# Optimization experiments

Hardware: AMD Instinct MI355X
Metric: run time of the kernel (lower is better)

## Reference

```python
import jax, jax.numpy as jnp
import numpy as np

B, S, H, D = 32, 2048, 1024, 1024
NEG_BIG = -1e10  # matches torch's -10000000000.0 sentinel


def setup_inputs() -> dict:
    key = jax.random.key(0)
    k1, k2, k3, k4, k5 = jax.random.split(key, 5)
    hidden = jax.random.normal(k1, (B, H), dtype=jnp.float32)
    encoder_outs = jax.random.normal(k2, (B, S, D), dtype=jnp.float32)
    src_lens = jax.random.randint(k3, (B,), 1, S + 1, dtype=jnp.int64 if jax.config.jax_enable_x64 else jnp.int32)
    W1 = jax.random.normal(k4, (D, H), dtype=jnp.float32) * (1.0 / np.sqrt(H))
    W2 = jax.random.normal(k5, (D, H + D), dtype=jnp.float32) * (1.0 / np.sqrt(H + D))
    return {"hidden": hidden, "encoder_outs": encoder_outs, "src_lens": src_lens, "W1": W1, "W2": W2}


def reference(hidden, encoder_outs, src_lens, W1, W2):
    # x = l1(hidden): (B, D)
    x = hidden @ W1.T
    # att_score: (B, S) (torch computes (S, B); we keep batch-major and transpose attn at the end)
    scores = jnp.einsum('bsd,bd->bs', encoder_outs, x)
    seq_len = encoder_outs.shape[1]
    mask = (jnp.arange(seq_len)[None, :] < src_lens[:, None]).astype(scores.dtype)  # (B, S)
    masked = mask * scores
    # torch quirk: exact zeros (masked OR genuinely-zero scores) -> -1e10
    masked = jnp.where(masked == 0.0, jnp.asarray(NEG_BIG, masked.dtype), masked)
    attn = jax.nn.softmax(masked, axis=1)  # softmax over seq dim (torch dim=0 of (S,B))
    ctx = jnp.einsum('bs,bsd->bd', attn, encoder_outs)  # weighted sum: (B, D)
    out = jnp.tanh(jnp.concatenate([ctx, hidden], axis=1) @ W2.T)  # (B, D)
    return out, attn.T  # attn returned as (S, B) to match torch
```

## Files before the change

kernel.cpp:

```cpp
#include <hip/hip_runtime.h>
#include <hip/hip_bf16.h>
#include <math.h>

#define BB 32
#define SS 2048
#define HH 1024
#define DD 1024
#define HD 2048
#define NSPLIT 32
#define KSPLIT 8
#define NEG_BIG -1e10f

__device__ __forceinline__ float wave_reduce_sum(float v) {
#pragma unroll
    for (int off = 32; off > 0; off >>= 1) v += __shfl_xor(v, off, 64);
    return v;
}

__device__ __forceinline__ float dot4(float4 a, float4 b) {
    return a.x * b.x + a.y * b.y + a.z * b.z + a.w * b.w;
}

__global__ __launch_bounds__(256) void k1_gemv_x(const float* __restrict__ hidden,
                                                 const float* __restrict__ W1,
                                                 float* __restrict__ x) {
    __shared__ float4 hs[16 * 256];
    int tid = threadIdx.x;
    int w = tid >> 6, lane = tid & 63;
    int d = blockIdx.x * 4 + w;
    const float4* wp = (const float4*)(W1 + (size_t)d * HH);
    float4 w0 = wp[lane], w1 = wp[lane + 64], w2 = wp[lane + 128], w3 = wp[lane + 192];
    const float4* hp = (const float4*)hidden;

    for (int half = 0; half < 2; ++half) {
        __syncthreads();
#pragma unroll
        for (int i = 0; i < 16; ++i) hs[i * 256 + tid] = hp[half * 4096 + i * 256 + tid];
        __syncthreads();
#pragma unroll 4
        for (int bl = 0; bl < 16; ++bl) {
            const float4* hb = hs + bl * 256;
            float s = dot4(hb[lane], w0) + dot4(hb[lane + 64], w1) +
                      dot4(hb[lane + 128], w2) + dot4(hb[lane + 192], w3);
            s = wave_reduce_sum(s);
            if (lane == 0) x[(half * 16 + bl) * DD + d] = s;
        }
    }
}

__global__ __launch_bounds__(512) void k2_fused(const float* __restrict__ enc,
                                                const float* __restrict__ x,
                                                const int* __restrict__ src_lens,
                                                float* __restrict__ scores,
                                                float* __restrict__ ctxp,
                                                float* __restrict__ m_part,
                                                float* __restrict__ l_part) {
    int b = blockIdx.x >> 5;
    int sp = blockIdx.x & 31;
    int tid = threadIdx.x;
    int w = tid >> 6, lane = tid & 63;
    int len = src_lens[b];
    int srow = sp * 64 + w * 8;

    float m = NEG_BIG, l = 0.f;
    float4 a0 = {0, 0, 0, 0}, a1 = {0, 0, 0, 0}, a2 = {0, 0, 0, 0}, a3 = {0, 0, 0, 0};

    if (srow < len) {
        const float4* xp = (const float4*)(x + (size_t)b * DD);
        float4 x0 = xp[lane], x1 = xp[lane + 64], x2 = xp[lane + 128], x3 = xp[lane + 192];
        int rend = min(8, len - srow);
        for (int r = 0; r < rend; ++r) {
            int s = srow + r;
            const float4* ep = (const float4*)(enc + ((size_t)b * SS + s) * DD);
            float4 e0 = ep[lane], e1 = ep[lane + 64], e2 = ep[lane + 128], e3 = ep[lane + 192];
            float part = dot4(e0, x0) + dot4(e1, x1) + dot4(e2, x2) + dot4(e3, x3);
            part = wave_reduce_sum(part);
            float v = part;
            if (v == 0.0f) v = NEG_BIG;
            if (lane == 0) scores[b * SS + s] = v;
            if (v > m) {
                float sc = __expf(m - v);
                m = v;
                l *= sc;
                a0.x *= sc; a0.y *= sc; a0.z *= sc; a0.w *= sc;
                a1.x *= sc; a1.y *= sc; a1.z *= sc; a1.w *= sc;
                a2.x *= sc; a2.y *= sc; a2.z *= sc; a2.w *= sc;
                a3.x *= sc; a3.y *= sc; a3.z *= sc; a3.w *= sc;
            }
            float p = __expf(v - m);
            l += p;
            a0.x += p * e0.x; a0.y += p * e0.y; a0.z += p * e0.z; a0.w += p * e0.w;
            a1.x += p * e1.x; a1.y += p * e1.y; a1.z += p * e1.z; a1.w += p * e1.w;
            a2.x += p * e2.x; a2.y += p * e2.y; a2.z += p * e2.z; a2.w += p * e2.w;
            a3.x += p * e3.x; a3.y += p * e3.y; a3.z += p * e3.z; a3.w += p * e3.w;
        }
    }
    {
        int s0 = max(srow, len);
        for (int s = s0 + lane; s < srow + 8; s += 64) scores[b * SS + s] = NEG_BIG;
    }

    __shared__ float4 lctx[8][256];
    __shared__ float lm[8], ll[8];
    lctx[w][lane] = a0;
    lctx[w][lane + 64] = a1;
    lctx[w][lane + 128] = a2;
    lctx[w][lane + 192] = a3;
    if (lane == 0) { lm[w] = m; ll[w] = l; }
    __syncthreads();

    if (tid < 256) {
        float M = lm[0];
#pragma unroll
        for (int k = 1; k < 8; ++k) M = fmaxf(M, lm[k]);
        float L = 0.f;
        float4 sum = {0, 0, 0, 0};
#pragma unroll
        for (int k = 0; k < 8; ++k) {
            float sc = __expf(lm[k] - M);
            L += sc * ll[k];
            float4 c = lctx[k][tid];
            sum.x += sc * c.x; sum.y += sc * c.y; sum.z += sc * c.z; sum.w += sc * c.w;
        }
        int cc = ((tid >> 6) << 8) | ((tid & 63) << 2);
        *(float4*)(ctxp + ((size_t)(b * NSPLIT + sp)) * DD + cc) = sum;
        if (tid == 0) {
            m_part[b * NSPLIT + sp] = M;
            l_part[b * NSPLIT + sp] = L;
        }
    }
}

__global__ __launch_bounds__(256) void k3_combine(const float* __restrict__ ctxp,
                                                  const float* __restrict__ m_part,
                                                  const float* __restrict__ l_part,
                                                  float* __restrict__ ctx,
                                                  float* __restrict__ Mb,
                                                  float* __restrict__ Lb) {
    int b = blockIdx.x;
    int tid = threadIdx.x;
    float M = -INFINITY;
#pragma unroll
    for (int k = 0; k < NSPLIT; ++k) M = fmaxf(M, m_part[b * NSPLIT + k]);
    float L = 0.f;
    float4 sum = {0, 0, 0, 0};
#pragma unroll
    for (int k = 0; k < NSPLIT; ++k) {
        float sc = __expf(m_part[b * NSPLIT + k] - M);
        L += sc * l_part[b * NSPLIT + k];
        float4 c = *(const float4*)(ctxp + ((size_t)(b * NSPLIT + k)) * DD + tid * 4);
        sum.x += sc * c.x; sum.y += sc * c.y; sum.z += sc * c.z; sum.w += sc * c.w;
    }
    float rL = 1.0f / L;
    float4 o = {sum.x * rL, sum.y * rL, sum.z * rL, sum.w * rL};
    *(float4*)(ctx + (size_t)b * DD + tid * 4) = o;
    if (tid == 0) { Mb[b] = M; Lb[b] = L; }
}

__global__ __launch_bounds__(256) void k5_outgemm(const float* __restrict__ ctx,
                                                  const float* __restrict__ hidden,
                                                  const float* __restrict__ W2,
                                                  float* __restrict__ outp) {
    int dt = blockIdx.x & 31;
    int ks = blockIdx.x >> 5;
    int tid = threadIdx.x;
    __shared__ float cat_s[32 * 128];
    __shared__ float w2_s[32 * 128];
    int b0 = tid & 15, b1 = b0 + 16;
    int dl0 = (tid >> 4) * 2, dl1 = dl0 + 1;
    float acc00 = 0.f, acc01 = 0.f, acc10 = 0.f, acc11 = 0.f;

    for (int c = 0; c < 2; ++c) {
        int j0 = ks * 256 + c * 128;
        __syncthreads();
#pragma unroll
        for (int pass = 0; pass < 4; ++pass) {
            int r = pass * 8 + (tid >> 5);
            int jj4 = tid & 31;
            int j = j0 + jj4 * 4;
            const float* src = (j < 1024) ? (ctx + (size_t)r * 1024 + j)
                                          : (hidden + (size_t)r * 1024 + (j - 1024));
            float4 v = *(const float4*)src;
            *(float4*)(cat_s + r * 128 + ((jj4 ^ (r & 7)) << 2)) = v;
            int dg = dt * 32 + r;
            float4 wv = *(const float4*)(W2 + (size_t)dg * HD + j);
            *(float4*)(w2_s + r * 128 + ((jj4 ^ (r & 7)) << 2)) = wv;
        }
        __syncthreads();
#pragma unroll 4
        for (int jj4 = 0; jj4 < 32; ++jj4) {
            float4 cA = *(const float4*)(cat_s + b0 * 128 + ((jj4 ^ (b0 & 7)) << 2));
            float4 cB = *(const float4*)(cat_s + b1 * 128 + ((jj4 ^ (b1 & 7)) << 2));
            float4 wA = *(const float4*)(w2_s + dl0 * 128 + ((jj4 ^ (dl0 & 7)) << 2));
            float4 wB = *(const float4*)(w2_s + dl1 * 128 + ((jj4 ^ (dl1 & 7)) << 2));
            acc00 += dot4(cA, wA);
            acc01 += dot4(cA, wB);
            acc10 += dot4(cB, wA);
            acc11 += dot4(cB, wB);
        }
    }
    float* op = outp + (size_t)ks * (BB * DD);
    op[b0 * 1024 + dt * 32 + dl0] = acc00;
    op[b0 * 1024 + dt * 32 + dl1] = acc01;
    op[b1 * 1024 + dt * 32 + dl0] = acc10;
    op[b1 * 1024 + dt * 32 + dl1] = acc11;
}

__global__ __launch_bounds__(256) void k6_final(const float* __restrict__ outp,
                                                const float* __restrict__ scores,
                                                const float* __restrict__ Mb,
                                                const float* __restrict__ Lb,
                                                float* __restrict__ out) {
    int i = blockIdx.x * 256 + threadIdx.x;
    if (i < BB * DD) {
        float s = 0.f;
#pragma unroll
        for (int k = 0; k < KSPLIT; ++k) s += outp[(size_t)k * (BB * DD) + i];
        out[i] = tanhf(s);
    } else {
        int j = i - BB * DD;
        int b = j & 31, sIdx = j >> 5;
        float v = __expf(scores[b * SS + sIdx] - Mb[b]) / Lb[b];
        out[i] = v;
    }
}

extern "C" void kernel_launch(void* const* d_in, const int* in_sizes, int n_in,
                              void* d_out, int out_size, void* d_ws, size_t ws_size,
                              hipStream_t stream) {
    const float* hidden = (const float*)d_in[0];
    const float* enc = (const float*)d_in[1];
    const int* src_lens = (const int*)d_in[2];
    const float* W1 = (const float*)d_in[3];
    const float* W2 = (const float*)d_in[4];
    float* out = (float*)d_out;
    float* ws = (float*)d_ws;

    float* x = ws;
    float* scores = ws + 32768;
    float* ctxp = ws + 98304;
    float* m_part = ws + 1146880;
    float* l_part = ws + 1147904;
    float* Mb = ws + 1148928;
    float* Lb = ws + 1148960;
    float* ctx = ws + 1148992;
    float* outp = ws + 1181760;

    k1_gemv_x<<<256, 256, 0, stream>>>(hidden, W1, x);
    k2_fused<<<1024, 512, 0, stream>>>(enc, x, src_lens, scores, ctxp, m_part, l_part);
    k3_combine<<<32, 256, 0, stream>>>(ctxp, m_part, l_part, ctx, Mb, Lb);
    k5_outgemm<<<256, 256, 0, stream>>>(ctx, hidden, W2, outp);
    k6_final<<<384, 256, 0, stream>>>(outp, scores, Mb, Lb, out);
}
```

Baseline: 59.95 us.

## Compact valid sequence chunks in attention kernel and widen combine/out-GEMM parallelism

The fused score/context kernel now builds a prefix sum of per-batch valid 64-row chunks and walks only those chunks with a grid-stride loop over 512 blocks. This replaces 1024 fixed blocks, many of which covered only padded rows. The combine kernel loops only over each batch's valid splits and uses four blocks per batch. The output GEMM doubles its K split to 16, giving 512 blocks with one tile each. Padded scores are no longer written; the final kernel instead emits zero attention for positions past src_len. Risks are a load-imbalance tail when the chunk count is slightly above the block count, and the extra partial-sum traffic from the larger K split.

```diff
diff --git a/kernel.cpp b/kernel.cpp
--- a/kernel.cpp
+++ b/kernel.cpp
@@ -8,7 +8,7 @@
 #define DD 1024
 #define HD 2048
 #define NSPLIT 32
-#define KSPLIT 8
+#define KSPLIT 16
 #define NEG_BIG -1e10f
 
 __device__ __forceinline__ float wave_reduce_sum(float v) {
@@ -55,106 +55,117 @@
                                                 float* __restrict__ ctxp,
                                                 float* __restrict__ m_part,
                                                 float* __restrict__ l_part) {
-    int b = blockIdx.x >> 5;
-    int sp = blockIdx.x & 31;
     int tid = threadIdx.x;
     int w = tid >> 6, lane = tid & 63;
-    int len = src_lens[b];
-    int srow = sp * 64 + w * 8;
-
-    float m = NEG_BIG, l = 0.f;
-    float4 a0 = {0, 0, 0, 0}, a1 = {0, 0, 0, 0}, a2 = {0, 0, 0, 0}, a3 = {0, 0, 0, 0};
-
-    if (srow < len) {
-        const float4* xp = (const float4*)(x + (size_t)b * DD);
-        float4 x0 = xp[lane], x1 = xp[lane + 64], x2 = xp[lane + 128], x3 = xp[lane + 192];
-        int rend = min(8, len - srow);
-        for (int r = 0; r < rend; ++r) {
-            int s = srow + r;
-            const float4* ep = (const float4*)(enc + ((size_t)b * SS + s) * DD);
-            float4 e0 = ep[lane], e1 = ep[lane + 64], e2 = ep[lane + 128], e3 = ep[lane + 192];
-            float part = dot4(e0, x0) + dot4(e1, x1) + dot4(e2, x2) + dot4(e3, x3);
-            part = wave_reduce_sum(part);
-            float v = part;
-            if (v == 0.0f) v = NEG_BIG;
-            if (lane == 0) scores[b * SS + s] = v;
-            if (v > m) {
-                float sc = __expf(m - v);
-                m = v;
-                l *= sc;
-                a0.x *= sc; a0.y *= sc; a0.z *= sc; a0.w *= sc;
-                a1.x *= sc; a1.y *= sc; a1.z *= sc; a1.w *= sc;
-                a2.x *= sc; a2.y *= sc; a2.z *= sc; a2.w *= sc;
-                a3.x *= sc; a3.y *= sc; a3.z *= sc; a3.w *= sc;
-            }
-            float p = __expf(v - m);
-            l += p;
-            a0.x += p * e0.x; a0.y += p * e0.y; a0.z += p * e0.z; a0.w += p * e0.w;
-            a1.x += p * e1.x; a1.y += p * e1.y; a1.z += p * e1.z; a1.w += p * e1.w;
-            a2.x += p * e2.x; a2.y += p * e2.y; a2.z += p * e2.z; a2.w += p * e2.w;
-            a3.x += p * e3.x; a3.y += p * e3.y; a3.z += p * e3.z; a3.w += p * e3.w;
-        }
-    }
-    {
-        int s0 = max(srow, len);
-        for (int s = s0 + lane; s < srow + 8; s += 64) scores[b * SS + s] = NEG_BIG;
-    }
-
+
+    __shared__ int pfx[BB + 1];
+    if (tid == 0) {
+        int a = 0;
+        pfx[0] = 0;
+#pragma unroll
+        for (int b = 0; b < BB; ++b) {
+            a += (src_lens[b] + 63) >> 6;
+            pfx[b + 1] = a;
+        }
+    }
     __shared__ float4 lctx[8][256];
     __shared__ float lm[8], ll[8];
-    lctx[w][lane] = a0;
-    lctx[w][lane + 64] = a1;
-    lctx[w][lane + 128] = a2;
-    lctx[w][lane + 192] = a3;
-    if (lane == 0) { lm[w] = m; ll[w] = l; }
     __syncthreads();
-
-    if (tid < 256) {
-        float M = lm[0];
-#pragma unroll
-        for (int k = 1; k < 8; ++k) M = fmaxf(M, lm[k]);
-        float L = 0.f;
-        float4 sum = {0, 0, 0, 0};
-#pragma unroll
-        for (int k = 0; k < 8; ++k) {
-            float sc = __expf(lm[k] - M);
-            L += sc * ll[k];
-            float4 c = lctx[k][tid];
-            sum.x += sc * c.x; sum.y += sc * c.y; sum.z += sc * c.z; sum.w += sc * c.w;
-        }
-        int cc = ((tid >> 6) << 8) | ((tid & 63) << 2);
-        *(float4*)(ctxp + ((size_t)(b * NSPLIT + sp)) * DD + cc) = sum;
-        if (tid == 0) {
-            m_part[b * NSPLIT + sp] = M;
-            l_part[b * NSPLIT + sp] = L;
-        }
+    int total = pfx[BB];
+
+    for (int chunk = blockIdx.x; chunk < total; chunk += gridDim.x) {
+        int b = 0;
+        while (pfx[b + 1] <= chunk) ++b;
+        int sp = chunk - pfx[b];
+        int len = src_lens[b];
+        int srow = sp * 64 + w * 8;
+
+        float m = NEG_BIG, l = 0.f;
+        float4 a0 = {0, 0, 0, 0}, a1 = {0, 0, 0, 0}, a2 = {0, 0, 0, 0}, a3 = {0, 0, 0, 0};
+
+        if (srow < len) {
+            const float4* xp = (const float4*)(x + (size_t)b * DD);
+            float4 x0 = xp[lane], x1 = xp[lane + 64], x2 = xp[lane + 128], x3 = xp[lane + 192];
+            int rend = min(8, len - srow);
+            for (int r = 0; r < rend; ++r) {
+                int s = srow + r;
+                const float4* ep = (const float4*)(enc + ((size_t)b * SS + s) * DD);
+                float4 e0 = ep[lane], e1 = ep[lane + 64], e2 = ep[lane + 128], e3 = ep[lane + 192];
+                float part = dot4(e0, x0) + dot4(e1, x1) + dot4(e2, x2) + dot4(e3, x3);
+                part = wave_reduce_sum(part);
+                float v = part;
+                if (v == 0.0f) v = NEG_BIG;
+                if (lane == 0) scores[b * SS + s] = v;
+                if (v > m) {
+                    float sc = __expf(m - v);
+                    m = v;
+                    l *= sc;
+                    a0.x *= sc; a0.y *= sc; a0.z *= sc; a0.w *= sc;
+                    a1.x *= sc; a1.y *= sc; a1.z *= sc; a1.w *= sc;
+                    a2.x *= sc; a2.y *= sc; a2.z *= sc; a2.w *= sc;
+                    a3.x *= sc; a3.y *= sc; a3.z *= sc; a3.w *= sc;
+                }
+                float p = __expf(v - m);
+                l += p;
+                a0.x += p * e0.x; a0.y += p * e0.y; a0.z += p * e0.z; a0.w += p * e0.w;
+                a1.x += p * e1.x; a1.y += p * e1.y; a1.z += p * e1.z; a1.w += p * e1.w;
+                a2.x += p * e2.x; a2.y += p * e2.y; a2.z += p * e2.z; a2.w += p * e2.w;
+                a3.x += p * e3.x; a3.y += p * e3.y; a3.z += p * e3.z; a3.w += p * e3.w;
+            }
+        }
+
+        lctx[w][lane] = a0;
+        lctx[w][lane + 64] = a1;
+        lctx[w][lane + 128] = a2;
+        lctx[w][lane + 192] = a3;
+        if (lane == 0) { lm[w] = m; ll[w] = l; }
+        __syncthreads();
+
+        if (tid < 256) {
+            float M = lm[0];
+#pragma unroll
+            for (int k = 1; k < 8; ++k) M = fmaxf(M, lm[k]);
+            float L = 0.f;
+            float4 sum = {0, 0, 0, 0};
+#pragma unroll
+            for (int k = 0; k < 8; ++k) {
+                float sc = __expf(lm[k] - M);
+                L += sc * ll[k];
+                float4 c = lctx[k][tid];
+                sum.x += sc * c.x; sum.y += sc * c.y; sum.z += sc * c.z; sum.w += sc * c.w;
+            }
+            int cc = ((tid >> 6) << 8) | ((tid & 63) << 2);
+            *(float4*)(ctxp + ((size_t)(b * NSPLIT + sp)) * DD + cc) = sum;
+            if (tid == 0) {
+                m_part[b * NSPLIT + sp] = M;
+                l_part[b * NSPLIT + sp] = L;
+            }
+        }
+        __syncthreads();
     }
 }
 
 __global__ __launch_bounds__(256) void k3_combine(const float* __restrict__ ctxp,
                                                   const float* __restrict__ m_part,
                                                   const float* __restrict__ l_part,
+                                                  const int* __restrict__ src_lens,
                                                   float* __restrict__ ctx,
                                                   float* __restrict__ Mb,
                                                   float* __restrict__ Lb) {
-    int b = blockIdx.x;
-    int tid = threadIdx.x;
-    float M = -INFINITY;
-#pragma unroll
-    for (int k = 0; k < NSPLIT; ++k) M = fmaxf(M, m_part[b * NSPLIT + k]);
+    int b = blockIdx.x >> 2;
+    int col = (blockIdx.x & 3) * 256 + threadIdx.x;
+    int nb = (src_lens[b] + 63) >> 6;
+    float M = NEG_BIG;
+    for (int k = 0; k < nb; ++k) M = fmaxf(M, m_part[b * NSPLIT + k]);
     float L = 0.f;
-    float4 sum = {0, 0, 0, 0};
-#pragma unroll
-    for (int k = 0; k < NSPLIT; ++k) {
+    float sum = 0.f;
+    for (int k = 0; k < nb; ++k) {
         float sc = __expf(m_part[b * NSPLIT + k] - M);
         L += sc * l_part[b * NSPLIT + k];
-        float4 c = *(const float4*)(ctxp + ((size_t)(b * NSPLIT + k)) * DD + tid * 4);
-        sum.x += sc * c.x; sum.y += sc * c.y; sum.z += sc * c.z; sum.w += sc * c.w;
-    }
-    float rL = 1.0f / L;
-    float4 o = {sum.x * rL, sum.y * rL, sum.z * rL, sum.w * rL};
-    *(float4*)(ctx + (size_t)b * DD + tid * 4) = o;
-    if (tid == 0) { Mb[b] = M; Lb[b] = L; }
+        sum += sc * ctxp[((size_t)(b * NSPLIT + k)) * DD + col];
+    }
+    ctx[(size_t)b * DD + col] = sum / L;
+    if (threadIdx.x == 0 && (blockIdx.x & 3) == 0) { Mb[b] = M; Lb[b] = L; }
 }
 
 __global__ __launch_bounds__(256) void k5_outgemm(const float* __restrict__ ctx,
@@ -170,34 +181,31 @@
     int dl0 = (tid >> 4) * 2, dl1 = dl0 + 1;
     float acc00 = 0.f, acc01 = 0.f, acc10 = 0.f, acc11 = 0.f;
 
-    for (int c = 0; c < 2; ++c) {
-        int j0 = ks * 256 + c * 128;
-        __syncthreads();
-#pragma unroll
-        for (int pass = 0; pass < 4; ++pass) {
-            int r = pass * 8 + (tid >> 5);
-            int jj4 = tid & 31;
-            int j = j0 + jj4 * 4;
-            const float* src = (j < 1024) ? (ctx + (size_t)r * 1024 + j)
-                                          : (hidden + (size_t)r * 1024 + (j - 1024));
-            float4 v = *(const float4*)src;
-            *(float4*)(cat_s + r * 128 + ((jj4 ^ (r & 7)) << 2)) = v;
-            int dg = dt * 32 + r;
-            float4 wv = *(const float4*)(W2 + (size_t)dg * HD + j);
-            *(float4*)(w2_s + r * 128 + ((jj4 ^ (r & 7)) << 2)) = wv;
-        }
-        __syncthreads();
+    int j0 = ks * 128;
+#pragma unroll
+    for (int pass = 0; pass < 4; ++pass) {
+        int r = pass * 8 + (tid >> 5);
+        int jj4 = tid & 31;
+        int j = j0 + jj4 * 4;
+        const float* src = (j < 1024) ? (ctx + (size_t)r * 1024 + j)
+                                      : (hidden + (size_t)r * 1024 + (j - 1024));
+        float4 v = *(const float4*)src;
+        *(float4*)(cat_s + r * 128 + ((jj4 ^ (r & 7)) << 2)) = v;
+        int dg = dt * 32 + r;
+        float4 wv = *(const float4*)(W2 + (size_t)dg * HD + j);
+        *(float4*)(w2_s + r * 128 + ((jj4 ^ (r & 7)) << 2)) = wv;
+    }
+    __syncthreads();
 #pragma unroll 4
-        for (int jj4 = 0; jj4 < 32; ++jj4) {
-            float4 cA = *(const float4*)(cat_s + b0 * 128 + ((jj4 ^ (b0 & 7)) << 2));
-            float4 cB = *(const float4*)(cat_s + b1 * 128 + ((jj4 ^ (b1 & 7)) << 2));
-            float4 wA = *(const float4*)(w2_s + dl0 * 128 + ((jj4 ^ (dl0 & 7)) << 2));
-            float4 wB = *(const float4*)(w2_s + dl1 * 128 + ((jj4 ^ (dl1 & 7)) << 2));
-            acc00 += dot4(cA, wA);
-            acc01 += dot4(cA, wB);
-            acc10 += dot4(cB, wA);
-            acc11 += dot4(cB, wB);
-        }
+    for (int jj4 = 0; jj4 < 32; ++jj4) {
+        float4 cA = *(const float4*)(cat_s + b0 * 128 + ((jj4 ^ (b0 & 7)) << 2));
+        float4 cB = *(const float4*)(cat_s + b1 * 128 + ((jj4 ^ (b1 & 7)) << 2));
+        float4 wA = *(const float4*)(w2_s + dl0 * 128 + ((jj4 ^ (dl0 & 7)) << 2));
+        float4 wB = *(const float4*)(w2_s + dl1 * 128 + ((jj4 ^ (dl1 & 7)) << 2));
+        acc00 += dot4(cA, wA);
+        acc01 += dot4(cA, wB);
+        acc10 += dot4(cB, wA);
+        acc11 += dot4(cB, wB);
     }
     float* op = outp + (size_t)ks * (BB * DD);
     op[b0 * 1024 + dt * 32 + dl0] = acc00;
@@ -208,6 +216,7 @@
 
 __global__ __launch_bounds__(256) void k6_final(const float* __restrict__ outp,
                                                 const float* __restrict__ scores,
+                                                const int* __restrict__ src_lens,
                                                 const float* __restrict__ Mb,
                                                 const float* __restrict__ Lb,
                                                 float* __restrict__ out) {
@@ -220,7 +229,8 @@
     } else {
         int j = i - BB * DD;
         int b = j & 31, sIdx = j >> 5;
-        float v = __expf(scores[b * SS + sIdx] - Mb[b]) / Lb[b];
+        float v = 0.0f;
+        if (sIdx < src_lens[b]) v = __expf(scores[b * SS + sIdx] - Mb[b]) / Lb[b];
         out[i] = v;
     }
 }
@@ -247,8 +257,8 @@
     float* outp = ws + 1181760;
 
     k1_gemv_x<<<256, 256, 0, stream>>>(hidden, W1, x);
-    k2_fused<<<1024, 512, 0, stream>>>(enc, x, src_lens, scores, ctxp, m_part, l_part);
-    k3_combine<<<32, 256, 0, stream>>>(ctxp, m_part, l_part, ctx, Mb, Lb);
-    k5_outgemm<<<256, 256, 0, stream>>>(ctx, hidden, W2, outp);
-    k6_final<<<384, 256, 0, stream>>>(outp, scores, Mb, Lb, out);
-}
+    k2_fused<<<512, 512, 0, stream>>>(enc, x, src_lens, scores, ctxp, m_part, l_part);
+    k3_combine<<<128, 256, 0, stream>>>(ctxp, m_part, l_part, src_lens, ctx, Mb, Lb);
+    k5_outgemm<<<512, 256, 0, stream>>>(ctx, hidden, W2, outp);
+    k6_final<<<384, 256, 0, stream>>>(outp, scores, src_lens, Mb, Lb, out);
+}
```

New measurement: 59.94 us. About the same (-0.0%).
